# Performance work log

Hardware: AMD Instinct MI355X
Metric: run time of the kernel (lower is better)

Reference implementation:

```python
import jax, jax.numpy as jnp
import numpy as np

G = 7          # grid size
OBJ_P = 0.3    # fraction of cells containing an object


def _to_xyxy(x, y, w, h, m, n):
    # x pairs with grid index m (dim 2), y with n (dim 3), per the original loop
    cx = (x + m) / G
    cy = (y + n) / G
    return cx - w / 2, cy - h / 2, cx + w / 2, cy + h / 2


def _iou(b1, b2):
    x1a, y1a, x2a, y2a = b1
    x1b, y1b, x2b, y2b = b2
    iw = jnp.maximum(jnp.minimum(x2a, x2b) - jnp.maximum(x1a, x1b), 0.0)
    ih = jnp.maximum(jnp.minimum(y2a, y2b) - jnp.maximum(y1a, y1b), 0.0)
    inter = iw * ih
    a1 = (x2a - x1a) * (y2a - y1a)
    a2 = (x2b - x1b) * (y2b - y1b)
    union = a1 + a2 - inter
    return jnp.where(inter > 0, inter / union, 0.0)


def setup_inputs() -> dict:
    key = jax.random.key(0)
    k1, k2, k3 = jax.random.split(key, 3)
    B = 32768
    pred = jax.random.uniform(k1, (B, 30, G, G), dtype=jnp.float32)
    labels = jax.random.uniform(k2, (B, 30, G, G), dtype=jnp.float32)
    obj_mask = jax.random.bernoulli(k3, OBJ_P, (B, G, G)).astype(jnp.float32)
    labels = labels.at[:, 4].set(obj_mask)
    return {"pred": pred, "labels": labels}


def reference(pred, labels):
    B = pred.shape[0]
    m = jnp.arange(G, dtype=pred.dtype)[:, None]   # dim 2
    n = jnp.arange(G, dtype=pred.dtype)[None, :]   # dim 3

    obj = labels[:, 4] == 1.0                       # (B,G,G)

    box1 = _to_xyxy(pred[:, 0], pred[:, 1], pred[:, 2], pred[:, 3], m, n)
    box2 = _to_xyxy(pred[:, 5], pred[:, 6], pred[:, 7], pred[:, 8], m, n)
    boxg = _to_xyxy(labels[:, 0], labels[:, 1], labels[:, 2], labels[:, 3], m, n)

    iou1 = _iou(box1, boxg)
    iou2 = _iou(box2, boxg)
    resp1 = iou1 >= iou2

    coor1 = 5.0 * (jnp.sum((pred[:, 0:2] - labels[:, 0:2]) ** 2, axis=1)
                   + jnp.sum((jnp.sqrt(pred[:, 2:4]) - jnp.sqrt(labels[:, 2:4])) ** 2, axis=1))
    coor2 = 5.0 * (jnp.sum((pred[:, 5:7] - labels[:, 5:7]) ** 2, axis=1)
                   + jnp.sum((jnp.sqrt(pred[:, 7:9]) - jnp.sqrt(labels[:, 7:9])) ** 2, axis=1))

    loss_b1 = coor1 + (pred[:, 4] - iou1) ** 2 + 0.5 * (pred[:, 9] - iou2) ** 2
    loss_b2 = coor2 + (pred[:, 9] - iou2) ** 2 + 0.5 * (pred[:, 4] - iou1) ** 2

    cls = jnp.sum((pred[:, 10:] - labels[:, 10:]) ** 2, axis=1)

    obj_loss = jnp.where(resp1, loss_b1, loss_b2) + cls
    noobj_loss = 0.5 * (pred[:, 4] ** 2 + pred[:, 9] ** 2)

    total = jnp.sum(jnp.where(obj, obj_loss, noobj_loss))
    return total / B
```

## Files before the change

### kernel.cpp

```cpp
#include <hip/hip_runtime.h>


#define GRID 7
#define NCH 30
#define CPI 49
#define FPI 1470
#define NBLK 2048
#define BLK 256

__device__ __forceinline__ float iou_xyxy(float x1a, float y1a, float x2a, float y2a,
                                          float x1b, float y1b, float x2b, float y2b) {
    float iw = fmaxf(fminf(x2a, x2b) - fmaxf(x1a, x1b), 0.0f);
    float ih = fmaxf(fminf(y2a, y2b) - fmaxf(y1a, y1b), 0.0f);
    float inter = iw * ih;
    float a1 = (x2a - x1a) * (y2a - y1a);
    float a2 = (x2b - x1b) * (y2b - y1b);
    float uni = a1 + a2 - inter;
    return inter > 0.0f ? inter / uni : 0.0f;
}

__device__ __forceinline__ void block_reduce_write(float acc, float* dst) {
    #pragma unroll
    for (int off = 32; off > 0; off >>= 1)
        acc += __shfl_down(acc, off, 64);
    __shared__ float rsm[4];
    int lane = threadIdx.x & 63;
    int wid = threadIdx.x >> 6;
    if (lane == 0) rsm[wid] = acc;
    __syncthreads();
    if (threadIdx.x == 0)
        dst[blockIdx.x] = rsm[0] + rsm[1] + rsm[2] + rsm[3];
}

__global__ void __launch_bounds__(BLK) yolo_partial_kernel(
        const float* __restrict__ pred,
        const float* __restrict__ labels,
        float* __restrict__ partials,
        int ncells, float invB) {
    float acc = 0.0f;
    int stride = gridDim.x * blockDim.x;

    for (int t = blockIdx.x * blockDim.x + threadIdx.x; t < ncells; t += stride) {
        int img = t / CPI;
        int cell = t - img * CPI;

        const float* pb = pred   + img * FPI + cell;
        const float* lb = labels + img * FPI + cell;

        float lobj = lb[4 * CPI];
        float p4 = pb[4 * CPI];
        float p9 = pb[9 * CPI];

        if (lobj == 1.0f) {
            int m = cell / GRID;
            int n = cell - m * GRID;
            float fm = (float)m, fn = (float)n;

            float p0 = pb[0 * CPI], p1 = pb[1 * CPI], p2 = pb[2 * CPI], p3 = pb[3 * CPI];
            float p5 = pb[5 * CPI], p6 = pb[6 * CPI], p7 = pb[7 * CPI], p8 = pb[8 * CPI];
            float l0 = lb[0 * CPI], l1 = lb[1 * CPI], l2 = lb[2 * CPI], l3 = lb[3 * CPI];
            float l5 = lb[5 * CPI], l6 = lb[6 * CPI], l7 = lb[7 * CPI], l8 = lb[8 * CPI];

            float cls = 0.0f;
            #pragma unroll
            for (int c = 10; c < NCH; ++c) {
                float d = pb[c * CPI] - lb[c * CPI];
                cls += d * d;
            }

            const float inv_g = 1.0f / (float)GRID;

            float cx = (p0 + fm) * inv_g, cy = (p1 + fn) * inv_g;
            float b1x1 = cx - p2 * 0.5f, b1y1 = cy - p3 * 0.5f;
            float b1x2 = cx + p2 * 0.5f, b1y2 = cy + p3 * 0.5f;
            cx = (p5 + fm) * inv_g; cy = (p6 + fn) * inv_g;
            float b2x1 = cx - p7 * 0.5f, b2y1 = cy - p8 * 0.5f;
            float b2x2 = cx + p7 * 0.5f, b2y2 = cy + p8 * 0.5f;
            cx = (l0 + fm) * inv_g; cy = (l1 + fn) * inv_g;
            float gx1 = cx - l2 * 0.5f, gy1 = cy - l3 * 0.5f;
            float gx2 = cx + l2 * 0.5f, gy2 = cy + l3 * 0.5f;

            float iou1 = iou_xyxy(b1x1, b1y1, b1x2, b1y2, gx1, gy1, gx2, gy2);
            float iou2 = iou_xyxy(b2x1, b2y1, b2x2, b2y2, gx1, gy1, gx2, gy2);
            bool resp1 = iou1 >= iou2;

            float dx = p0 - l0, dy = p1 - l1;
            float dw = sqrtf(p2) - sqrtf(l2), dh = sqrtf(p3) - sqrtf(l3);
            float coor1 = 5.0f * (dx * dx + dy * dy + dw * dw + dh * dh);
            dx = p5 - l5; dy = p6 - l6;
            dw = sqrtf(p7) - sqrtf(l7); dh = sqrtf(p8) - sqrtf(l8);
            float coor2 = 5.0f * (dx * dx + dy * dy + dw * dw + dh * dh);

            float e1 = p4 - iou1, e2 = p9 - iou2;
            float loss_b1 = coor1 + e1 * e1 + 0.5f * e2 * e2;
            float loss_b2 = coor2 + e2 * e2 + 0.5f * e1 * e1;

            acc += (resp1 ? loss_b1 : loss_b2) + cls;
        } else {
            acc += 0.5f * (p4 * p4 + p9 * p9);
        }
    }
    block_reduce_write(acc * invB, partials);
}

__global__ void __launch_bounds__(256) yolo_final_kernel(
        const float* __restrict__ partials, float* __restrict__ out, int np) {
    float acc = 0.0f;
    for (int i = threadIdx.x; i < np; i += 256)
        acc += partials[i];
    #pragma unroll
    for (int off = 32; off > 0; off >>= 1)
        acc += __shfl_down(acc, off, 64);
    __shared__ float rsm[4];
    int lane = threadIdx.x & 63;
    int wid = threadIdx.x >> 6;
    if (lane == 0) rsm[wid] = acc;
    __syncthreads();
    if (threadIdx.x == 0)
        out[0] = rsm[0] + rsm[1] + rsm[2] + rsm[3];
}

extern "C" void kernel_launch(void* const* d_in, const int* in_sizes, int n_in,
                              void* d_out, int out_size, void* d_ws, size_t ws_size,
                              hipStream_t stream) {
    const float* pred = (const float*)d_in[0];
    const float* labels = (const float*)d_in[1];
    float* out = (float*)d_out;
    float* partials = (float*)d_ws;

    int total = in_sizes[0];
    int B = total / FPI;
    if (B <= 0) return;
    float invB = 1.0f / (float)B;
    int ncells = B * CPI;

    int nblk = NBLK;
    size_t cap = ws_size / sizeof(float);
    if ((size_t)nblk > cap) nblk = (int)cap > 0 ? (int)cap : 1;

    yolo_partial_kernel<<<nblk, BLK, 0, stream>>>(pred, labels, partials,
                                                  ncells, invB);
    yolo_final_kernel<<<1, 256, 0, stream>>>(partials, out, nblk);
}
```

Before: 382.6 us.

## Process four cells per thread with float4 loads and branchless loss

Each thread now handles a group of four adjacent grid cells (plus a tail item for cell 48), loading each channel row as an unaligned 16-byte vector instead of scalar strided loads. The per-cell loss is computed branchlessly with a select on the object flag, so all channels are always read and all arithmetic always executed. This aims to raise memory-level parallelism and remove wave divergence, at the cost of more registers, unaligned vector accesses and an unbalanced tail item per image.

```diff
diff --git a/kernel.cpp b/kernel.cpp
--- a/kernel.cpp
+++ b/kernel.cpp
@@ -5,8 +5,18 @@
 #define NCH 30
 #define CPI 49
 #define FPI 1470
+#define IPT 13
+#define BLK 256
 #define NBLK 2048
-#define BLK 256
+
+__device__ __forceinline__ float4 ld4u(const float* p) {
+    float4 v;
+    __builtin_memcpy(&v, p, 16);
+    return v;
+}
+__device__ __forceinline__ float elem(const float4& v, int k) {
+    return ((const float*)&v)[k];
+}
 
 __device__ __forceinline__ float iou_xyxy(float x1a, float y1a, float x2a, float y2a,
                                           float x1b, float y1b, float x2b, float y2b) {
@@ -17,6 +27,44 @@
     float a2 = (x2b - x1b) * (y2b - y1b);
     float uni = a1 + a2 - inter;
     return inter > 0.0f ? inter / uni : 0.0f;
+}
+
+__device__ __forceinline__ float cell_loss_s(
+        float p0, float p1, float p2, float p3, float p4,
+        float p5, float p6, float p7, float p8, float p9,
+        float l0, float l1, float l2, float l3, float lobj,
+        float l5, float l6, float l7, float l8,
+        float cls, float fm, float fn) {
+    const float inv_g = 1.0f / (float)GRID;
+
+    float cx = (p0 + fm) * inv_g, cy = (p1 + fn) * inv_g;
+    float b1x1 = cx - p2 * 0.5f, b1y1 = cy - p3 * 0.5f;
+    float b1x2 = cx + p2 * 0.5f, b1y2 = cy + p3 * 0.5f;
+    cx = (p5 + fm) * inv_g; cy = (p6 + fn) * inv_g;
+    float b2x1 = cx - p7 * 0.5f, b2y1 = cy - p8 * 0.5f;
+    float b2x2 = cx + p7 * 0.5f, b2y2 = cy + p8 * 0.5f;
+    cx = (l0 + fm) * inv_g; cy = (l1 + fn) * inv_g;
+    float gx1 = cx - l2 * 0.5f, gy1 = cy - l3 * 0.5f;
+    float gx2 = cx + l2 * 0.5f, gy2 = cy + l3 * 0.5f;
+
+    float iou1 = iou_xyxy(b1x1, b1y1, b1x2, b1y2, gx1, gy1, gx2, gy2);
+    float iou2 = iou_xyxy(b2x1, b2y1, b2x2, b2y2, gx1, gy1, gx2, gy2);
+    bool resp1 = iou1 >= iou2;
+
+    float dx = p0 - l0, dy = p1 - l1;
+    float dw = sqrtf(p2) - sqrtf(l2), dh = sqrtf(p3) - sqrtf(l3);
+    float coor1 = 5.0f * (dx * dx + dy * dy + dw * dw + dh * dh);
+    dx = p5 - l5; dy = p6 - l6;
+    dw = sqrtf(p7) - sqrtf(l7); dh = sqrtf(p8) - sqrtf(l8);
+    float coor2 = 5.0f * (dx * dx + dy * dy + dw * dw + dh * dh);
+
+    float e1 = p4 - iou1, e2 = p9 - iou2;
+    float loss_b1 = coor1 + e1 * e1 + 0.5f * e2 * e2;
+    float loss_b2 = coor2 + e2 * e2 + 0.5f * e1 * e1;
+
+    float obj_loss = (resp1 ? loss_b1 : loss_b2) + cls;
+    float noobj_loss = 0.5f * (p4 * p4 + p9 * p9);
+    return (lobj == 1.0f) ? obj_loss : noobj_loss;
 }
 
 __device__ __forceinline__ void block_reduce_write(float acc, float* dst) {
@@ -36,68 +84,65 @@
         const float* __restrict__ pred,
         const float* __restrict__ labels,
         float* __restrict__ partials,
-        int ncells, float invB) {
+        int nitems, float invB) {
     float acc = 0.0f;
     int stride = gridDim.x * blockDim.x;
 
-    for (int t = blockIdx.x * blockDim.x + threadIdx.x; t < ncells; t += stride) {
-        int img = t / CPI;
-        int cell = t - img * CPI;
+    for (int t = blockIdx.x * blockDim.x + threadIdx.x; t < nitems; t += stride) {
+        int img = t / IPT;
+        int item = t - img * IPT;
+        const float* pb0 = pred   + img * FPI;
+        const float* lb0 = labels + img * FPI;
 
-        const float* pb = pred   + img * FPI + cell;
-        const float* lb = labels + img * FPI + cell;
+        if (item < 12) {
+            int c0 = item * 4;
+            const float* pb = pb0 + c0;
+            const float* lb = lb0 + c0;
 
-        float lobj = lb[4 * CPI];
-        float p4 = pb[4 * CPI];
-        float p9 = pb[9 * CPI];
+            float4 P[10], L[9];
+            #pragma unroll
+            for (int c = 0; c < 10; ++c) P[c] = ld4u(pb + c * CPI);
+            #pragma unroll
+            for (int c = 0; c < 9; ++c)  L[c] = ld4u(lb + c * CPI);
 
-        if (lobj == 1.0f) {
-            int m = cell / GRID;
-            int n = cell - m * GRID;
-            float fm = (float)m, fn = (float)n;
+            float4 cls4 = make_float4(0.f, 0.f, 0.f, 0.f);
+            #pragma unroll
+            for (int c = 10; c < NCH; ++c) {
+                float4 pv = ld4u(pb + c * CPI);
+                float4 lv = ld4u(lb + c * CPI);
+                float dx = pv.x - lv.x, dy = pv.y - lv.y;
+                float dz = pv.z - lv.z, dw = pv.w - lv.w;
+                cls4.x += dx * dx; cls4.y += dy * dy;
+                cls4.z += dz * dz; cls4.w += dw * dw;
+            }
 
-            float p0 = pb[0 * CPI], p1 = pb[1 * CPI], p2 = pb[2 * CPI], p3 = pb[3 * CPI];
-            float p5 = pb[5 * CPI], p6 = pb[6 * CPI], p7 = pb[7 * CPI], p8 = pb[8 * CPI];
-            float l0 = lb[0 * CPI], l1 = lb[1 * CPI], l2 = lb[2 * CPI], l3 = lb[3 * CPI];
-            float l5 = lb[5 * CPI], l6 = lb[6 * CPI], l7 = lb[7 * CPI], l8 = lb[8 * CPI];
-
+            #pragma unroll
+            for (int k = 0; k < 4; ++k) {
+                int cell = c0 + k;
+                int m = cell / GRID;
+                int n = cell - m * GRID;
+                acc += cell_loss_s(
+                    elem(P[0],k), elem(P[1],k), elem(P[2],k), elem(P[3],k), elem(P[4],k),
+                    elem(P[5],k), elem(P[6],k), elem(P[7],k), elem(P[8],k), elem(P[9],k),
+                    elem(L[0],k), elem(L[1],k), elem(L[2],k), elem(L[3],k), elem(L[4],k),
+                    elem(L[5],k), elem(L[6],k), elem(L[7],k), elem(L[8],k),
+                    elem(cls4,k), (float)m, (float)n);
+            }
+        } else {
+            const float* pb = pb0 + 48;
+            const float* lb = lb0 + 48;
             float cls = 0.0f;
             #pragma unroll
             for (int c = 10; c < NCH; ++c) {
                 float d = pb[c * CPI] - lb[c * CPI];
                 cls += d * d;
             }
-
-            const float inv_g = 1.0f / (float)GRID;
-
-            float cx = (p0 + fm) * inv_g, cy = (p1 + fn) * inv_g;
-            float b1x1 = cx - p2 * 0.5f, b1y1 = cy - p3 * 0.5f;
-            float b1x2 = cx + p2 * 0.5f, b1y2 = cy + p3 * 0.5f;
-            cx = (p5 + fm) * inv_g; cy = (p6 + fn) * inv_g;
-            float b2x1 = cx - p7 * 0.5f, b2y1 = cy - p8 * 0.5f;
-            float b2x2 = cx + p7 * 0.5f, b2y2 = cy + p8 * 0.5f;
-            cx = (l0 + fm) * inv_g; cy = (l1 + fn) * inv_g;
-            float gx1 = cx - l2 * 0.5f, gy1 = cy - l3 * 0.5f;
-            float gx2 = cx + l2 * 0.5f, gy2 = cy + l3 * 0.5f;
-
-            float iou1 = iou_xyxy(b1x1, b1y1, b1x2, b1y2, gx1, gy1, gx2, gy2);
-            float iou2 = iou_xyxy(b2x1, b2y1, b2x2, b2y2, gx1, gy1, gx2, gy2);
-            bool resp1 = iou1 >= iou2;
-
-            float dx = p0 - l0, dy = p1 - l1;
-            float dw = sqrtf(p2) - sqrtf(l2), dh = sqrtf(p3) - sqrtf(l3);
-            float coor1 = 5.0f * (dx * dx + dy * dy + dw * dw + dh * dh);
-            dx = p5 - l5; dy = p6 - l6;
-            dw = sqrtf(p7) - sqrtf(l7); dh = sqrtf(p8) - sqrtf(l8);
-            float coor2 = 5.0f * (dx * dx + dy * dy + dw * dw + dh * dh);
-
-            float e1 = p4 - iou1, e2 = p9 - iou2;
-            float loss_b1 = coor1 + e1 * e1 + 0.5f * e2 * e2;
-            float loss_b2 = coor2 + e2 * e2 + 0.5f * e1 * e1;
-
-            acc += (resp1 ? loss_b1 : loss_b2) + cls;
-        } else {
-            acc += 0.5f * (p4 * p4 + p9 * p9);
+            acc += cell_loss_s(
+                pb[0*CPI], pb[1*CPI], pb[2*CPI], pb[3*CPI], pb[4*CPI],
+                pb[5*CPI], pb[6*CPI], pb[7*CPI], pb[8*CPI], pb[9*CPI],
+                lb[0*CPI], lb[1*CPI], lb[2*CPI], lb[3*CPI], lb[4*CPI],
+                lb[5*CPI], lb[6*CPI], lb[7*CPI], lb[8*CPI],
+                cls, 6.0f, 6.0f);
         }
     }
     block_reduce_write(acc * invB, partials);
@@ -132,13 +177,13 @@
     int B = total / FPI;
     if (B <= 0) return;
     float invB = 1.0f / (float)B;
-    int ncells = B * CPI;
+    int nitems = B * IPT;
 
     int nblk = NBLK;
     size_t cap = ws_size / sizeof(float);
     if ((size_t)nblk > cap) nblk = (int)cap > 0 ? (int)cap : 1;
 
     yolo_partial_kernel<<<nblk, BLK, 0, stream>>>(pred, labels, partials,
-                                                  ncells, invB);
+                                                  nitems, invB);
     yolo_final_kernel<<<1, 256, 0, stream>>>(partials, out, nblk);
 }
```

Measured after the change: 397.1 us. +3.8%, slower.
